# Optimization experiments

Measured on AMD Instinct MI355X. Metric: run time of the kernel, lower is better.

## Reference

```python
import jax, jax.numpy as jnp
import numpy as np

B, C, H, W = 8, 256, 64, 64
N = 3  # num_param
EPS = 1e-5


def conv2d(x, w, b=None, stride=(1, 1), padding=((0, 0), (0, 0)), dilation=(1, 1), groups=1):
    out = jax.lax.conv_general_dilated(
        x, w, window_strides=stride, padding=padding, rhs_dilation=dilation,
        dimension_numbers=('NCHW', 'OIHW', 'NCHW'), feature_group_count=groups)
    if b is not None:
        out = out + b[None, :, None, None]
    return out


def akconv(x, p_w, p_b, ak_w, ak_gamma, ak_beta):
    b, c, h, w = x.shape
    offset = conv2d(x, p_w, p_b, padding=((1, 1), (1, 1)))  # (b, 2N, h, w)
    # initial kernel offsets p_n for num_param=3: rows [0,0,1], cols [0,1,0]
    p_n = jnp.concatenate([jnp.array([0., 0., 1.]), jnp.array([0., 1., 0.])]).reshape(1, 2 * N, 1, 1)
    gx = jnp.broadcast_to(jnp.arange(h, dtype=x.dtype)[:, None], (h, w))
    gy = jnp.broadcast_to(jnp.arange(w, dtype=x.dtype)[None, :], (h, w))
    p_0 = jnp.concatenate([jnp.tile(gx[None, None], (1, N, 1, 1)),
                           jnp.tile(gy[None, None], (1, N, 1, 1))], axis=1)  # (1, 2N, h, w)
    p = p_0 + p_n + offset                      # (b, 2N, h, w)
    p = jnp.transpose(p, (0, 2, 3, 1))          # (b, h, w, 2N)
    q = jnp.floor(jax.lax.stop_gradient(p))
    q_lt_x = jnp.clip(q[..., :N], 0, h - 1)
    q_lt_y = jnp.clip(q[..., N:], 0, w - 1)
    q_rb_x = jnp.clip(q[..., :N] + 1, 0, h - 1)
    q_rb_y = jnp.clip(q[..., N:] + 1, 0, w - 1)
    px = jnp.clip(p[..., :N], 0, h - 1)
    py = jnp.clip(p[..., N:], 0, w - 1)
    # bilinear weights (b, h, w, N)
    g_lt = (1 + (q_lt_x - px)) * (1 + (q_lt_y - py))
    g_rb = (1 - (q_rb_x - px)) * (1 - (q_rb_y - py))
    g_lb = (1 + (q_lt_x - px)) * (1 - (q_rb_y - py))
    g_rt = (1 - (q_rb_x - px)) * (1 + (q_lt_y - py))

    x_flat = x.reshape(b, c, h * w)

    def gather(qx, qy):
        idx = (qx * w + qy).astype(jnp.int32).reshape(b, -1)  # (b, h*w*N)
        out = jnp.take_along_axis(x_flat, idx[:, None, :], axis=2)
        return out.reshape(b, c, h, w, N)

    x_off = (g_lt[:, None] * gather(q_lt_x, q_lt_y)
             + g_rb[:, None] * gather(q_rb_x, q_rb_y)
             + g_lb[:, None] * gather(q_lt_x, q_rb_y)
             + g_rt[:, None] * gather(q_rb_x, q_lt_y))   # (b, c, h, w, N)
    # rearrange 'b c h w n -> b c (h n) w'
    x_off = jnp.transpose(x_off, (0, 1, 2, 4, 3)).reshape(b, c, h * N, w)
    out = conv2d(x_off, ak_w, None, stride=(N, 1))        # (b, c, h, w)
    # BatchNorm2d in training mode (batch statistics) + SiLU
    mean = out.mean(axis=(0, 2, 3), keepdims=True)
    var = ((out - mean) ** 2).mean(axis=(0, 2, 3), keepdims=True)
    out = (out - mean) / jnp.sqrt(var + EPS) * ak_gamma[None, :, None, None] + ak_beta[None, :, None, None]
    return jax.nn.silu(out)


def lka(x, w0, b0, ws, bs, w1, b1):
    u = x
    attn = conv2d(x, w0, b0, padding=((2, 2), (2, 2)), groups=C)                       # 5x5 depthwise
    attn = conv2d(attn, ws, bs, padding=((9, 9), (9, 9)), dilation=(3, 3), groups=C)   # 7x7 dw, dil 3
    attn = conv2d(attn, w1, b1)                                                        # 1x1
    return u * attn


def setup_inputs() -> dict:
    key = jax.random.key(0)
    ks = jax.random.split(key, 8)
    return {
        'x': jax.random.normal(ks[0], (B, C, H, W), jnp.float32),
        'p_w': jax.random.normal(ks[1], (2 * N, C, 3, 3), jnp.float32) * 0.01,
        'p_b': jnp.zeros((2 * N,), jnp.float32),
        'ak_w': jax.random.normal(ks[2], (C, C, 3, 1), jnp.float32) * 0.05,
        'ak_gamma': jnp.ones((C,), jnp.float32),
        'ak_beta': jnp.zeros((C,), jnp.float32),
        'lka0_w': jax.random.normal(ks[3], (C, 1, 5, 5), jnp.float32) * 0.05,
        'lka0_b': jnp.zeros((C,), jnp.float32),
        'lkas_w': jax.random.normal(ks[4], (C, 1, 7, 7), jnp.float32) * 0.05,
        'lkas_b': jnp.zeros((C,), jnp.float32),
        'lka1_w': jax.random.normal(ks[5], (C, C, 1, 1), jnp.float32) * 0.05,
        'lka1_b': jnp.zeros((C,), jnp.float32),
        'conv_w': jax.random.normal(ks[6], (C, C, 1, 1), jnp.float32) * 0.05,
        'conv_b': jnp.zeros((C,), jnp.float32),
    }


def reference(x, p_w, p_b, ak_w, ak_gamma, ak_beta, lka0_w, lka0_b, lkas_w, lkas_b, lka1_w, lka1_b, conv_w, conv_b):
    res = x
    y = akconv(x, p_w, p_b, ak_w, ak_gamma, ak_beta)
    y = lka(y, lka0_w, lka0_b, lkas_w, lkas_b, lka1_w, lka1_b)
    y = conv2d(y, conv_w, conv_b)
    return y + res
```

## Files before the change

kernel.cpp:

```cpp
#include <hip/hip_runtime.h>
#include <math.h>
#include <stdint.h>

#define B_ 8
#define C_ 256
#define HW_ 4096
#define NPIX 32768
#define NELEM (B_*C_*HW_)

typedef __attribute__((ext_vector_type(8))) short short8;
typedef __attribute__((ext_vector_type(4))) float f32x4;

__device__ __forceinline__ unsigned short f2bf(float f) {
    union { float f; uint32_t u; } v; v.f = f;
    uint32_t r = v.u + 0x7FFFu + ((v.u >> 16) & 1u);
    return (unsigned short)(r >> 16);
}
__device__ __forceinline__ float b2f(unsigned short h) {
    union { uint32_t u; float f; } v; v.u = ((uint32_t)h) << 16; return v.f;
}
__device__ __forceinline__ float silu_f(float v) { return v / (1.f + __expf(-v)); }

__global__ __launch_bounds__(256) void prep_kernel(
    const float* __restrict__ akw, const float* __restrict__ l1w,
    const float* __restrict__ cvw, const float* __restrict__ pw,
    unsigned short* __restrict__ wak, unsigned short* __restrict__ wl1,
    unsigned short* __restrict__ wcv, float* __restrict__ pwt)
{
    int gid = blockIdx.x * 256 + threadIdx.x;
    if (gid < 196608) {
        unsigned co = (unsigned)gid / 768u;
        unsigned kp = (unsigned)gid - co * 768u;
        unsigned n = kp >> 8, ci = kp & 255;
        wak[gid] = f2bf(akw[co * 768 + ci * 3 + n]);
    }
    else if (gid < 262144) { int g = gid - 196608; wl1[g] = f2bf(l1w[g]); }
    else if (gid < 327680) { int g = gid - 262144; wcv[g] = f2bf(cvw[g]); }
    else if (gid < 346112) {
        int idx = gid - 327680;
        int ci = idx / 72, r = idx - ci * 72;
        int tt = r / 12, t9 = r - tt * 12;
        pwt[idx] = (t9 < 9) ? pw[tt * 2304 + ci * 9 + t9] : 0.f;
    }
}

__global__ __launch_bounds__(256) void transpose_kernel(
    const float* __restrict__ x, float* __restrict__ xt)
{
    int blk = blockIdx.x;
    int b = blk & 7;
    int rest = blk >> 3;
    int half = rest & 1, i = rest >> 1;
    int bi = b * 64 + i;
    int tid = threadIdx.x;
    __shared__ float tile[64 * 132];

    {
        int ci_l = tid >> 6, jj = tid & 63;
        const float* ip = x + ((size_t)b * C_ + half * 128 + ci_l) * HW_ + i * 64 + jj;
        #pragma unroll 4
        for (int it = 0; it < 32; ++it)
            tile[jj * 132 + ci_l + it * 4] = ip[(size_t)it * 4 * HW_];
    }
    __syncthreads();
    {
        int j = tid >> 2, q = tid & 3;
        float* op = xt + ((size_t)(bi * 64 + j)) * 256 + half * 128 + q * 32;
        #pragma unroll
        for (int f = 0; f < 8; ++f)
            *(float4*)(op + f * 4) = *(const float4*)&tile[j * 132 + q * 32 + f * 4];
    }
}

__global__ __launch_bounds__(256) void offset_s1_kernel(
    const float* __restrict__ x, const float* __restrict__ pwt,
    float* __restrict__ part)
{
    int blk = blockIdx.x;
    int b = blk & 7;
    int rest = blk >> 3;
    int g = rest & 7, i = rest >> 3;
    int bi = b * 64 + i;
    int tid = threadIdx.x;

    __shared__ float tile[6600];

    {
        int cs = tid >> 3, r8 = tid & 7;
        const float* xp = x + ((size_t)b * C_ + g * 32 + cs) * HW_;
        #pragma unroll
        for (int t = 0; t < 6; ++t) {
            int idx = r8 * 6 + t;
            int r = idx >> 4, v4 = idx & 15;
            int ii = i + r - 1;
            float4 val = make_float4(0.f, 0.f, 0.f, 0.f);
            if (ii >= 0 && ii < 64)
                val = *(const float4*)(xp + ii * 64 + v4 * 4);
            int base = (r * 66 + 1 + v4 * 4) * 33 + cs;
            tile[base]      = val.x;  tile[base + 33]  = val.y;
            tile[base + 66] = val.z;  tile[base + 99]  = val.w;
        }
        if (tid < 192) {
            int ci = tid / 6, rem = tid - ci * 6;
            int ki = rem >> 1, side = rem & 1;
            tile[(ki * 66 + side * 65) * 33 + ci] = 0.f;
        }
    }
    __syncthreads();

    int sub = tid >> 4;
    int jq  = tid & 15;

    float acc[6][4];
    #pragma unroll
    for (int tt = 0; tt < 6; ++tt)
        #pragma unroll
        for (int p = 0; p < 4; ++p) acc[tt][p] = 0.f;

    #pragma unroll
    for (int t = 0; t < 2; ++t) {
        int ci = sub + 16 * t;
        float xv[3][6];
        #pragma unroll
        for (int ki = 0; ki < 3; ++ki)
            #pragma unroll
            for (int cc = 0; cc < 6; ++cc)
                xv[ki][cc] = tile[(ki * 66 + jq * 4 + cc) * 33 + ci];
        const float* wp = pwt + (g * 32 + ci) * 72;
        #pragma unroll
        for (int tt = 0; tt < 6; ++tt) {
            float w[9];
            *(float4*)&w[0] = *(const float4*)(wp + tt * 12);
            *(float4*)&w[4] = *(const float4*)(wp + tt * 12 + 4);
            w[8] = wp[tt * 12 + 8];
            #pragma unroll
            for (int ki = 0; ki < 3; ++ki)
                #pragma unroll
                for (int kj = 0; kj < 3; ++kj) {
                    float wgt = w[ki * 3 + kj];
                    #pragma unroll
                    for (int p = 0; p < 4; ++p)
                        acc[tt][p] += wgt * xv[ki][kj + p];
                }
        }
    }

    __syncthreads();
    {
        float* s2 = tile + sub * 387;
        #pragma unroll
        for (int tt = 0; tt < 6; ++tt)
            #pragma unroll
            for (int p = 0; p < 4; ++p)
                s2[tt * 64 + jq * 4 + p] = acc[tt][p];
    }
    __syncthreads();
    size_t pslot = (size_t)bi * 8 + g;
    for (int idx = tid; idx < 384; idx += 256) {
        float s = 0.f;
        #pragma unroll
        for (int sb = 0; sb < 16; ++sb)
            s += tile[sb * 387 + idx];
        part[pslot * 384 + idx] = s;
    }
}

__global__ __launch_bounds__(256) void offset_s2_kernel(
    const float* __restrict__ part, const float* __restrict__ pb,
    int2* __restrict__ tbl_off, float4* __restrict__ tbl_w)
{
    int pix = blockIdx.x * 256 + threadIdx.x;
    int b = pix >> 12, rem = pix & 4095, i = rem >> 6, j = rem & 63;
    int bi = b * 64 + i;
    float v[6];
    #pragma unroll
    for (int tt = 0; tt < 6; ++tt) v[tt] = pb[tt];
    for (int g = 0; g < 8; ++g) {
        const float* pp = part + ((size_t)bi * 8 + g) * 384;
        #pragma unroll
        for (int tt = 0; tt < 6; ++tt) v[tt] += pp[tt * 64 + j];
    }
    const float pnx[3] = {0.f, 0.f, 1.f};
    const float pny[3] = {0.f, 1.f, 0.f};
    #pragma unroll
    for (int n = 0; n < 3; ++n) {
        float px_ = (float)i + pnx[n] + v[n];
        float py_ = (float)j + pny[n] + v[n + 3];
        float qx = floorf(px_), qy = floorf(py_);
        float qlx = fminf(fmaxf(qx,       0.f), 63.f);
        float qly = fminf(fmaxf(qy,       0.f), 63.f);
        float qrx = fminf(fmaxf(qx + 1.f, 0.f), 63.f);
        float qry = fminf(fmaxf(qy + 1.f, 0.f), 63.f);
        float pxc = fminf(fmaxf(px_,      0.f), 63.f);
        float pyc = fminf(fmaxf(py_,      0.f), 63.f);
        float glt = (1.f + (qlx - pxc)) * (1.f + (qly - pyc));
        float grb = (1.f - (qrx - pxc)) * (1.f - (qry - pyc));
        float glb = (1.f + (qlx - pxc)) * (1.f - (qry - pyc));
        float grt = (1.f - (qrx - pxc)) * (1.f + (qly - pyc));
        int ilx = (int)qlx, irx = (int)qrx;
        int ily = (int)qly, iry = (int)qry;
        int c0; float a0, a1, b0, b1;
        if (ily == iry) {
            if (ily == 0) { c0 = 0;  a0 = glt + glb; a1 = 0.f; b0 = grt + grb; b1 = 0.f; }
            else          { c0 = 62; a0 = 0.f; a1 = glt + glb; b0 = 0.f; b1 = grt + grb; }
        } else { c0 = ily; a0 = glt; a1 = glb; b0 = grt; b1 = grb; }
        int oi = (b * 3 + n) * HW_ + i * 64 + j;
        tbl_off[oi] = make_int2(ilx * 64 + c0, irx * 64 + c0);
        tbl_w[oi]   = make_float4(a0, a1, b0, b1);
    }
}

__global__ __launch_bounds__(256) void gather_kernel(
    const float* __restrict__ xt, const int2* __restrict__ tbl_off,
    const float4* __restrict__ tbl_w, unsigned short* __restrict__ v)
{
    int blk = blockIdx.x;
    int b = blk & 7;
    int rest = blk >> 3;
    int n = rest >> 6, i = rest & 63;
    int bi = b * 64 + i;
    int tid = threadIdx.x;
    int lane = tid & 63, wv = tid >> 6;
    int ci4 = lane * 4;
    const float* xb = xt + (size_t)b * 1048576;

    for (int it0 = 0; it0 < 16; it0 += 4) {
        float4 A[4], Bv[4], Cv[4], Dv[4], w4[4];
        #pragma unroll
        for (int u = 0; u < 4; ++u) {
            int j = wv * 16 + it0 + u;
            int oi = (b * 3 + n) * HW_ + i * 64 + j;
            int2 off = tbl_off[oi];
            w4[u] = tbl_w[oi];
            const float* p0 = xb + (size_t)off.x * 256 + ci4;
            const float* p1 = xb + (size_t)off.y * 256 + ci4;
            A[u]  = *(const float4*)p0;
            Bv[u] = *(const float4*)(p0 + 256);
            Cv[u] = *(const float4*)p1;
            Dv[u] = *(const float4*)(p1 + 256);
        }
        #pragma unroll
        for (int u = 0; u < 4; ++u) {
            int j = wv * 16 + it0 + u;
            int pix = bi * 64 + j;
            union { unsigned short h[4]; uint2 q; } pk;
            pk.h[0] = f2bf(w4[u].x*A[u].x + w4[u].y*Bv[u].x + w4[u].z*Cv[u].x + w4[u].w*Dv[u].x);
            pk.h[1] = f2bf(w4[u].x*A[u].y + w4[u].y*Bv[u].y + w4[u].z*Cv[u].y + w4[u].w*Dv[u].y);
            pk.h[2] = f2bf(w4[u].x*A[u].z + w4[u].y*Bv[u].z + w4[u].z*Cv[u].z + w4[u].w*Dv[u].z);
            pk.h[3] = f2bf(w4[u].x*A[u].w + w4[u].y*Bv[u].w + w4[u].z*Cv[u].w + w4[u].w*Dv[u].w);
            *(uint2*)&v[(size_t)pix * 768 + n * 256 + ci4] = pk.q;
        }
    }
}

__global__ __launch_bounds__(256) void ak_mfma_kernel(
    const unsigned short* __restrict__ v, const unsigned short* __restrict__ W,
    unsigned short* __restrict__ yh, float* __restrict__ p1, float* __restrict__ p2)
{
    int blk = blockIdx.x;
    int b = blk & 7, i = blk >> 3;
    int tid = threadIdx.x;
    int wv = tid >> 6, lane = tid & 63;
    int quad = lane >> 4, l15 = lane & 15;
    __shared__ __align__(16) unsigned short sA[8192];
    __shared__ __align__(16) unsigned short sB[2048];
    int pixS = tid & 63, kqS = tid >> 6;
    int pix0 = (b * 64 + i) * 64;

    f32x4 acc[4][4];
    #pragma unroll
    for (int mt = 0; mt < 4; ++mt)
        #pragma unroll
        for (int nt = 0; nt < 4; ++nt) acc[mt][nt] = (f32x4){0.f, 0.f, 0.f, 0.f};

    for (int k0 = 0; k0 < 768; k0 += 32) {
        #pragma unroll
        for (int s = 0; s < 4; ++s) {
            int co = tid;
            *(uint4*)&sA[(s * 256 + co) * 8] =
                *(const uint4*)&W[co * 768 + k0 + s * 8];
        }
        *(uint4*)&sB[(kqS * 64 + pixS) * 8] =
            *(const uint4*)&v[(size_t)(pix0 + pixS) * 768 + k0 + kqS * 8];
        __syncthreads();
        short8 af[4], bf[4];
        #pragma unroll
        for (int mt = 0; mt < 4; ++mt)
            af[mt] = *(const short8*)&sA[(quad * 256 + wv * 64 + mt * 16 + l15) * 8];
        #pragma unroll
        for (int nt = 0; nt < 4; ++nt)
            bf[nt] = *(const short8*)&sB[(quad * 64 + nt * 16 + l15) * 8];
        #pragma unroll
        for (int mt = 0; mt < 4; ++mt)
            #pragma unroll
            for (int nt = 0; nt < 4; ++nt)
                acc[mt][nt] = __builtin_amdgcn_mfma_f32_16x16x32_bf16(
                    af[mt], bf[nt], acc[mt][nt], 0, 0, 0);
        __syncthreads();
    }
    #pragma unroll
    for (int mt = 0; mt < 4; ++mt) {
        #pragma unroll
        for (int r = 0; r < 4; ++r) {
            int co = wv * 64 + mt * 16 + quad * 4 + r;
            size_t base = ((size_t)b * C_ + co) * HW_ + i * 64;
            float s1 = 0.f, s2 = 0.f;
            #pragma unroll
            for (int nt = 0; nt < 4; ++nt) {
                float val = acc[mt][nt][r];
                s1 += val; s2 += val * val;
                yh[base + nt * 16 + l15] = f2bf(val);
            }
            #pragma unroll
            for (int m = 1; m < 16; m <<= 1) {
                s1 += __shfl_xor(s1, m); s2 += __shfl_xor(s2, m);
            }
            if (l15 == 0) { p1[co * 512 + blk] = s1; p2[co * 512 + blk] = s2; }
        }
    }
}

__global__ __launch_bounds__(256) void bn_stats_kernel(
    const float* __restrict__ p1, const float* __restrict__ p2,
    const float* __restrict__ gamma, const float* __restrict__ beta,
    float* __restrict__ ss)
{
    int co = blockIdx.x, tid = threadIdx.x;
    float a = p1[co * 512 + tid] + p1[co * 512 + 256 + tid];
    float q = p2[co * 512 + tid] + p2[co * 512 + 256 + tid];
    __shared__ float r1[256], r2[256];
    r1[tid] = a; r2[tid] = q; __syncthreads();
    for (int st = 128; st > 0; st >>= 1) {
        if (tid < st) { r1[tid] += r1[tid + st]; r2[tid] += r2[tid + st]; }
        __syncthreads();
    }
    if (tid == 0) {
        const float inv_n = 1.f / (float)NPIX;
        float m = r1[0] * inv_n;
        float var = r2[0] * inv_n - m * m;
        float sc = gamma[co] * rsqrtf(var + 1e-5f);
        ss[co] = sc; ss[256 + co] = beta[co] - m * sc;
    }
}

__global__ __launch_bounds__(256) void dw5_fused_kernel(
    const unsigned short* __restrict__ in, const float* __restrict__ ss,
    const float* __restrict__ w, const float* __restrict__ bias,
    unsigned short* __restrict__ out)
{
    int blkI = blockIdx.x;
    int b = blkI & 7, c = blkI >> 3;
    int bc = b * 256 + c;
    int tid = threadIdx.x;
    __shared__ float tile[68 * 68];
    float sc = ss[c], sh = ss[256 + c];
    const unsigned short* ip = in + (size_t)bc * HW_;
    for (int s = tid; s < 68 * 68; s += 256) {
        int r = s / 68, cc = s - r * 68;
        int ii = r - 2, jj = cc - 2;
        float vv = 0.f;
        if (ii >= 0 && ii < 64 && jj >= 0 && jj < 64) {
            float t = b2f(ip[ii * 64 + jj]) * sc + sh;
            vv = silu_f(t);
        }
        tile[s] = vv;
    }
    float wr[25];
    #pragma unroll
    for (int t = 0; t < 25; ++t) wr[t] = w[c * 25 + t];
    float bv = bias[c];
    __syncthreads();
    int j0 = (tid & 15) * 4, ig = tid >> 4;
    unsigned short* op = out + (size_t)bc * HW_;
    for (int r = 0; r < 4; ++r) {
        int i = r * 16 + ig;
        float o0 = bv, o1 = bv, o2 = bv, o3 = bv;
        #pragma unroll
        for (int di = 0; di < 5; ++di) {
            const float* tp = &tile[(i + di) * 68 + j0];
            float4 a = *(const float4*)tp;
            float4 bq = *(const float4*)(tp + 4);
            float vv[8] = {a.x, a.y, a.z, a.w, bq.x, bq.y, bq.z, bq.w};
            #pragma unroll
            for (int dj = 0; dj < 5; ++dj) {
                float wv = wr[di * 5 + dj];
                o0 += wv * vv[dj];     o1 += wv * vv[dj + 1];
                o2 += wv * vv[dj + 2]; o3 += wv * vv[dj + 3];
            }
        }
        union { unsigned short h[4]; uint2 u; } pk;
        pk.h[0] = f2bf(o0); pk.h[1] = f2bf(o1);
        pk.h[2] = f2bf(o2); pk.h[3] = f2bf(o3);
        *(uint2*)&op[i * 64 + j0] = pk.u;
    }
}

__global__ __launch_bounds__(256) void dw7d3_kernel(
    const unsigned short* __restrict__ in, const float* __restrict__ w,
    const float* __restrict__ bias, unsigned short* __restrict__ out)
{
    int blkI = blockIdx.x;
    int b = blkI & 7, c = blkI >> 3;
    int bc = b * 256 + c;
    int tid = threadIdx.x;
    __shared__ float tile[82 * 84];
    const unsigned short* ip = in + (size_t)bc * HW_;
    for (int s = tid; s < 82 * 84; s += 256) {
        int r = s / 84, cc = s - r * 84;
        int ii = r - 9, jj = cc - 9;
        float vv = 0.f;
        if (ii >= 0 && ii < 64 && jj >= 0 && jj < 64) vv = b2f(ip[ii * 64 + jj]);
        tile[s] = vv;
    }
    float wr[49];
    #pragma unroll
    for (int t = 0; t < 49; ++t) wr[t] = w[c * 49 + t];
    float bv = bias[c];
    __syncthreads();
    int j0 = (tid & 15) * 4, ig = tid >> 4;
    unsigned short* op = out + (size_t)bc * HW_;
    for (int r = 0; r < 4; ++r) {
        int i = r * 16 + ig;
        float o0 = bv, o1 = bv, o2 = bv, o3 = bv;
        #pragma unroll
        for (int di = 0; di < 7; ++di) {
            const float* tp = &tile[(i + 3 * di) * 84 + j0];
            float vv[24];
            #pragma unroll
            for (int q = 0; q < 6; ++q)
                *(float4*)&vv[q * 4] = *(const float4*)(tp + q * 4);
            #pragma unroll
            for (int dj = 0; dj < 7; ++dj) {
                float wv = wr[di * 7 + dj];
                o0 += wv * vv[3 * dj];     o1 += wv * vv[3 * dj + 1];
                o2 += wv * vv[3 * dj + 2]; o3 += wv * vv[3 * dj + 3];
            }
        }
        union { unsigned short h[4]; uint2 u; } pk;
        pk.h[0] = f2bf(o0); pk.h[1] = f2bf(o1);
        pk.h[2] = f2bf(o2); pk.h[3] = f2bf(o3);
        *(uint2*)&op[i * 64 + j0] = pk.u;
    }
}

template<int MODE>
__global__ __launch_bounds__(256) void gemm1x1_mfma(
    const unsigned short* __restrict__ in, const unsigned short* __restrict__ W,
    const float* __restrict__ bias,
    const unsigned short* __restrict__ auxh, const float* __restrict__ auxf,
    const float* __restrict__ ss,
    unsigned short* __restrict__ out_bf, float* __restrict__ out_f)
{
    int blk = blockIdx.x;
    int b = blk & 7, i = blk >> 3;
    int tid = threadIdx.x;
    int wv = tid >> 6, lane = tid & 63;
    int quad = lane >> 4, l15 = lane & 15;
    __shared__ __align__(16) unsigned short sA[8192];
    __shared__ __align__(16) unsigned short sB[2048];
    int pixS = tid & 63, kqS = tid >> 6;

    f32x4 acc[4][4];
    #pragma unroll
    for (int mt = 0; mt < 4; ++mt)
        #pragma unroll
        for (int nt = 0; nt < 4; ++nt) acc[mt][nt] = (f32x4){0.f, 0.f, 0.f, 0.f};

    for (int k0 = 0; k0 < 256; k0 += 32) {
        #pragma unroll
        for (int s = 0; s < 4; ++s) {
            int co = tid;
            *(uint4*)&sA[(s * 256 + co) * 8] =
                *(const uint4*)&W[co * 256 + k0 + s * 8];
        }
        {
            const unsigned short* vp =
                in + ((size_t)b * C_ + k0 + kqS * 8) * HW_ + i * 64 + pixS;
            union { unsigned short h[8]; uint4 u; } hb;
            #pragma unroll
            for (int jj = 0; jj < 8; ++jj) hb.h[jj] = vp[(size_t)jj * HW_];
            *(uint4*)&sB[(kqS * 64 + pixS) * 8] = hb.u;
        }
        __syncthreads();
        short8 af[4], bf[4];
        #pragma unroll
        for (int mt = 0; mt < 4; ++mt)
            af[mt] = *(const short8*)&sA[(quad * 256 + wv * 64 + mt * 16 + l15) * 8];
        #pragma unroll
        for (int nt = 0; nt < 4; ++nt)
            bf[nt] = *(const short8*)&sB[(quad * 64 + nt * 16 + l15) * 8];
        #pragma unroll
        for (int mt = 0; mt < 4; ++mt)
            #pragma unroll
            for (int nt = 0; nt < 4; ++nt)
                acc[mt][nt] = __builtin_amdgcn_mfma_f32_16x16x32_bf16(
                    af[mt], bf[nt], acc[mt][nt], 0, 0, 0);
        __syncthreads();
    }
    #pragma unroll
    for (int mt = 0; mt < 4; ++mt) {
        #pragma unroll
        for (int r = 0; r < 4; ++r) {
            int co = wv * 64 + mt * 16 + quad * 4 + r;
            float bco = bias[co];
            size_t base = ((size_t)b * C_ + co) * HW_ + i * 64;
            if (MODE == 0) {
                float sc = ss[co], sh = ss[256 + co];
                #pragma unroll
                for (int nt = 0; nt < 4; ++nt) {
                    int col = nt * 16 + l15;
                    float o = acc[mt][nt][r] + bco;
                    float u = silu_f(b2f(auxh[base + col]) * sc + sh);
                    out_bf[base + col] = f2bf(o * u);
                }
            } else {
                #pragma unroll
                for (int nt = 0; nt < 4; ++nt) {
                    int col = nt * 16 + l15;
                    out_f[base + col] = acc[mt][nt][r] + bco + auxf[base + col];
                }
            }
        }
    }
}

extern "C" void kernel_launch(void* const* d_in, const int* in_sizes, int n_in,
                              void* d_out, int out_size, void* d_ws, size_t ws_size,
                              hipStream_t stream) {
    const float* x     = (const float*)d_in[0];
    const float* p_w   = (const float*)d_in[1];
    const float* p_b   = (const float*)d_in[2];
    const float* ak_w  = (const float*)d_in[3];
    const float* ak_g  = (const float*)d_in[4];
    const float* ak_b  = (const float*)d_in[5];
    const float* l0_w  = (const float*)d_in[6];
    const float* l0_b  = (const float*)d_in[7];
    const float* ls_w  = (const float*)d_in[8];
    const float* ls_b  = (const float*)d_in[9];
    const float* l1_w  = (const float*)d_in[10];
    const float* l1_b  = (const float*)d_in[11];
    const float* cv_w  = (const float*)d_in[12];
    const float* cv_b  = (const float*)d_in[13];
    float* out = (float*)d_out;

    char* w = (char*)d_ws;
    int2*   tbl_off = (int2*)w;
    float4* tbl_w   = (float4*)(w + 786432);
    unsigned short* wak = (unsigned short*)(w + 2359296);
    unsigned short* wl1 = (unsigned short*)(w + 2752512);
    unsigned short* wcv = (unsigned short*)(w + 2883584);
    float* p1 = (float*)(w + 3014656);
    float* p2 = (float*)(w + 3538944);
    float* ss = (float*)(w + 4063232);
    float* pwt = (float*)(w + 4065280);
    float* xt   = (float*)(w + 4194304);
    unsigned short* ybh    = (unsigned short*)(w + 4194304);
    unsigned short* dw5out = (unsigned short*)(w + 20971520);
    float* part = (float*)(w + 37748736);
    unsigned short* attn   = (unsigned short*)(w + 37748736);
    unsigned short* v      = (unsigned short*)(w + 44040192);
    unsigned short* g0out  = (unsigned short*)(w + 54525952);

    prep_kernel<<<1352, 256, 0, stream>>>(ak_w, l1_w, cv_w, p_w, wak, wl1, wcv, pwt);
    offset_s1_kernel<<<4096, 256, 0, stream>>>(x, pwt, part);
    offset_s2_kernel<<<128, 256, 0, stream>>>(part, p_b, tbl_off, tbl_w);
    transpose_kernel<<<1024, 256, 0, stream>>>(x, xt);
    gather_kernel<<<1536, 256, 0, stream>>>(xt, tbl_off, tbl_w, v);
    ak_mfma_kernel<<<512, 256, 0, stream>>>(v, wak, ybh, p1, p2);
    bn_stats_kernel<<<256, 256, 0, stream>>>(p1, p2, ak_g, ak_b, ss);
    dw5_fused_kernel<<<2048, 256, 0, stream>>>(ybh, ss, l0_w, l0_b, dw5out);
    dw7d3_kernel<<<2048, 256, 0, stream>>>(dw5out, ls_w, ls_b, attn);
    gemm1x1_mfma<0><<<512, 256, 0, stream>>>(attn, wl1, l1_b, ybh, nullptr, ss, g0out, nullptr);
    gemm1x1_mfma<1><<<512, 256, 0, stream>>>(g0out, wcv, cv_b, nullptr, x, nullptr, nullptr, out);
}
```

Before: 316.8 us.

## Double-buffer GEMM tiles with direct global-to-LDS loads in AK and 1x1 kernels

Converts the AK-conv GEMM and the 1x1 GEMM kernels to a double-buffered LDS pipeline. Each loop iteration now issues the next K-slice while MFMAs run on the current one, using global_load_lds to copy weights (and AK activations) straight into shared memory without going through registers. The 1x1 kernel keeps a register-staged strided B load that is written to LDS after the compute. This doubles LDS use per block, which may lower occupancy, and depends on the LDS layout produced by the per-wave global_load_lds matching the old indexing.

Result: slower. 342.1 us (+8.0%).

```diff
diff --git a/kernel.cpp b/kernel.cpp
--- a/kernel.cpp
+++ b/kernel.cpp
@@ -20,6 +20,18 @@
     union { uint32_t u; float f; } v; v.u = ((uint32_t)h) << 16; return v.f;
 }
 __device__ __forceinline__ float silu_f(float v) { return v / (1.f + __expf(-v)); }
+
+__device__ __forceinline__ void gl2lds16(const void* g, void* l) {
+    __builtin_amdgcn_global_load_lds(
+        (const __attribute__((address_space(1))) void*)g,
+        (__attribute__((address_space(3))) void*)l,
+        16, 0, 0);
+}
+__device__ __forceinline__ void pipeline_barrier() {
+    asm volatile("s_waitcnt vmcnt(0) lgkmcnt(0)" ::: "memory");
+    __builtin_amdgcn_s_barrier();
+    asm volatile("" ::: "memory");
+}
 
 __global__ __launch_bounds__(256) void prep_kernel(
     const float* __restrict__ akw, const float* __restrict__ l1w,
@@ -262,41 +274,47 @@
     int tid = threadIdx.x;
     int wv = tid >> 6, lane = tid & 63;
     int quad = lane >> 4, l15 = lane & 15;
-    __shared__ __align__(16) unsigned short sA[8192];
-    __shared__ __align__(16) unsigned short sB[2048];
-    int pixS = tid & 63, kqS = tid >> 6;
+    __shared__ __align__(16) unsigned short sA[2][8192];
+    __shared__ __align__(16) unsigned short sB[2][2048];
     int pix0 = (b * 64 + i) * 64;
 
+    const unsigned short* wp = W + (size_t)(wv * 64 + lane) * 768;
+    const unsigned short* vp = v + (size_t)(pix0 + lane) * 768;
+
     f32x4 acc[4][4];
     #pragma unroll
     for (int mt = 0; mt < 4; ++mt)
         #pragma unroll
         for (int nt = 0; nt < 4; ++nt) acc[mt][nt] = (f32x4){0.f, 0.f, 0.f, 0.f};
 
-    for (int k0 = 0; k0 < 768; k0 += 32) {
-        #pragma unroll
-        for (int s = 0; s < 4; ++s) {
-            int co = tid;
-            *(uint4*)&sA[(s * 256 + co) * 8] =
-                *(const uint4*)&W[co * 768 + k0 + s * 8];
-        }
-        *(uint4*)&sB[(kqS * 64 + pixS) * 8] =
-            *(const uint4*)&v[(size_t)(pix0 + pixS) * 768 + k0 + kqS * 8];
-        __syncthreads();
+    auto stage = [&](int bb, int k0) {
+        #pragma unroll
+        for (int s = 0; s < 4; ++s)
+            gl2lds16(wp + k0 + s * 8, &sA[bb][(s * 256 + wv * 64) * 8]);
+        gl2lds16(vp + k0 + wv * 8, &sB[bb][(wv * 64) * 8]);
+    };
+
+    stage(0, 0);
+    pipeline_barrier();
+    int cur = 0;
+    #pragma unroll 2
+    for (int t = 0; t < 24; ++t) {
+        if (t < 23) stage(cur ^ 1, (t + 1) * 32);
         short8 af[4], bf[4];
         #pragma unroll
         for (int mt = 0; mt < 4; ++mt)
-            af[mt] = *(const short8*)&sA[(quad * 256 + wv * 64 + mt * 16 + l15) * 8];
+            af[mt] = *(const short8*)&sA[cur][(quad * 256 + wv * 64 + mt * 16 + l15) * 8];
         #pragma unroll
         for (int nt = 0; nt < 4; ++nt)
-            bf[nt] = *(const short8*)&sB[(quad * 64 + nt * 16 + l15) * 8];
+            bf[nt] = *(const short8*)&sB[cur][(quad * 64 + nt * 16 + l15) * 8];
         #pragma unroll
         for (int mt = 0; mt < 4; ++mt)
             #pragma unroll
             for (int nt = 0; nt < 4; ++nt)
                 acc[mt][nt] = __builtin_amdgcn_mfma_f32_16x16x32_bf16(
                     af[mt], bf[nt], acc[mt][nt], 0, 0, 0);
-        __syncthreads();
+        pipeline_barrier();
+        cur ^= 1;
     }
     #pragma unroll
     for (int mt = 0; mt < 4; ++mt) {
@@ -456,46 +474,61 @@
     int tid = threadIdx.x;
     int wv = tid >> 6, lane = tid & 63;
     int quad = lane >> 4, l15 = lane & 15;
-    __shared__ __align__(16) unsigned short sA[8192];
-    __shared__ __align__(16) unsigned short sB[2048];
+    __shared__ __align__(16) unsigned short sA[2][8192];
+    __shared__ __align__(16) unsigned short sB[2][2048];
     int pixS = tid & 63, kqS = tid >> 6;
 
+    const unsigned short* wp = W + (size_t)(wv * 64 + lane) * 256;
+    const unsigned short* bp = in + ((size_t)b * C_) * HW_ + i * 64 + pixS;
+
     f32x4 acc[4][4];
     #pragma unroll
     for (int mt = 0; mt < 4; ++mt)
         #pragma unroll
         for (int nt = 0; nt < 4; ++nt) acc[mt][nt] = (f32x4){0.f, 0.f, 0.f, 0.f};
 
-    for (int k0 = 0; k0 < 256; k0 += 32) {
-        #pragma unroll
-        for (int s = 0; s < 4; ++s) {
-            int co = tid;
-            *(uint4*)&sA[(s * 256 + co) * 8] =
-                *(const uint4*)&W[co * 256 + k0 + s * 8];
-        }
-        {
-            const unsigned short* vp =
-                in + ((size_t)b * C_ + k0 + kqS * 8) * HW_ + i * 64 + pixS;
-            union { unsigned short h[8]; uint4 u; } hb;
-            #pragma unroll
-            for (int jj = 0; jj < 8; ++jj) hb.h[jj] = vp[(size_t)jj * HW_];
-            *(uint4*)&sB[(kqS * 64 + pixS) * 8] = hb.u;
-        }
-        __syncthreads();
+    auto stageA = [&](int bb, int k0) {
+        #pragma unroll
+        for (int s = 0; s < 4; ++s)
+            gl2lds16(wp + k0 + s * 8, &sA[bb][(s * 256 + wv * 64) * 8]);
+    };
+    union U8 { unsigned short h[8]; uint4 u; };
+    auto loadB = [&](U8& hb, int k0) {
+        const unsigned short* p = bp + (size_t)(k0 + kqS * 8) * HW_;
+        #pragma unroll
+        for (int jj = 0; jj < 8; ++jj) hb.h[jj] = p[(size_t)jj * HW_];
+    };
+
+    U8 hb;
+    stageA(0, 0);
+    loadB(hb, 0);
+    asm volatile("s_waitcnt vmcnt(0)" ::: "memory");
+    *(uint4*)&sB[0][(kqS * 64 + pixS) * 8] = hb.u;
+    pipeline_barrier();
+
+    int cur = 0;
+    #pragma unroll 2
+    for (int t = 0; t < 8; ++t) {
+        if (t < 7) { stageA(cur ^ 1, (t + 1) * 32); loadB(hb, (t + 1) * 32); }
         short8 af[4], bf[4];
         #pragma unroll
         for (int mt = 0; mt < 4; ++mt)
-            af[mt] = *(const short8*)&sA[(quad * 256 + wv * 64 + mt * 16 + l15) * 8];
+            af[mt] = *(const short8*)&sA[cur][(quad * 256 + wv * 64 + mt * 16 + l15) * 8];
         #pragma unroll
         for (int nt = 0; nt < 4; ++nt)
-            bf[nt] = *(const short8*)&sB[(quad * 64 + nt * 16 + l15) * 8];
+            bf[nt] = *(const short8*)&sB[cur][(quad * 64 + nt * 16 + l15) * 8];
         #pragma unroll
         for (int mt = 0; mt < 4; ++mt)
             #pragma unroll
             for (int nt = 0; nt < 4; ++nt)
                 acc[mt][nt] = __builtin_amdgcn_mfma_f32_16x16x32_bf16(
                     af[mt], bf[nt], acc[mt][nt], 0, 0, 0);
-        __syncthreads();
+        if (t < 7) {
+            asm volatile("s_waitcnt vmcnt(0)" ::: "memory");
+            *(uint4*)&sB[cur ^ 1][(kqS * 64 + pixS) * 8] = hb.u;
+        }
+        pipeline_barrier();
+        cur ^= 1;
     }
     #pragma unroll
     for (int mt = 0; mt < 4; ++mt) {
```

## Split GEMM output channels across two blocks and load tiles via global_load_lds

Applied to the files above, without the earlier changes.

Each MFMA GEMM kernel (the AKConv 768-K GEMM and both 1x1 GEMMs) now covers half the output channels per block, which doubles the grid from 512 to 1024 blocks and halves accumulator registers and weight LDS. The weight and activation tile loads switch to direct global-to-LDS transfers, which skip the VGPR round-trip. The aim is better occupancy and latency hiding on a 256-CU part. In exchange, the B tile (pixels) is now loaded twice across the two blocks, and per-block MFMA work per sync is halved.

After: 326.1 us. 2.9% more time.

```diff
diff --git a/kernel.cpp b/kernel.cpp
--- a/kernel.cpp
+++ b/kernel.cpp
@@ -20,6 +20,13 @@
     union { uint32_t u; float f; } v; v.u = ((uint32_t)h) << 16; return v.f;
 }
 __device__ __forceinline__ float silu_f(float v) { return v / (1.f + __expf(-v)); }
+
+__device__ __forceinline__ void gl2lds16(const void* g, void* l) {
+    __builtin_amdgcn_global_load_lds(
+        (const __attribute__((address_space(1))) void*)g,
+        (__attribute__((address_space(3))) void*)l,
+        16, 0, 0);
+}
 
 __global__ __launch_bounds__(256) void prep_kernel(
     const float* __restrict__ akw, const float* __restrict__ l1w,
@@ -258,40 +265,45 @@
     unsigned short* __restrict__ yh, float* __restrict__ p1, float* __restrict__ p2)
 {
     int blk = blockIdx.x;
-    int b = blk & 7, i = blk >> 3;
+    int mt2 = blk & 1;
+    int rest = blk >> 1;
+    int b = rest & 7, i = rest >> 3;
     int tid = threadIdx.x;
     int wv = tid >> 6, lane = tid & 63;
     int quad = lane >> 4, l15 = lane & 15;
-    __shared__ __align__(16) unsigned short sA[8192];
+    __shared__ __align__(16) unsigned short sA[4096];
     __shared__ __align__(16) unsigned short sB[2048];
+    int pix0 = (b * 64 + i) * 64;
+    int co0 = mt2 * 128;
+
+    int coS = tid & 127, shS = tid >> 7;
     int pixS = tid & 63, kqS = tid >> 6;
-    int pix0 = (b * 64 + i) * 64;
-
-    f32x4 acc[4][4];
-    #pragma unroll
-    for (int mt = 0; mt < 4; ++mt)
+    const unsigned short* wpA = W + (size_t)(co0 + coS) * 768;
+    const unsigned short* vpB = v + (size_t)(pix0 + pixS) * 768;
+
+    f32x4 acc[2][4];
+    #pragma unroll
+    for (int mt = 0; mt < 2; ++mt)
         #pragma unroll
         for (int nt = 0; nt < 4; ++nt) acc[mt][nt] = (f32x4){0.f, 0.f, 0.f, 0.f};
 
     for (int k0 = 0; k0 < 768; k0 += 32) {
         #pragma unroll
-        for (int s = 0; s < 4; ++s) {
-            int co = tid;
-            *(uint4*)&sA[(s * 256 + co) * 8] =
-                *(const uint4*)&W[co * 768 + k0 + s * 8];
-        }
-        *(uint4*)&sB[(kqS * 64 + pixS) * 8] =
-            *(const uint4*)&v[(size_t)(pix0 + pixS) * 768 + k0 + kqS * 8];
+        for (int q = 0; q < 2; ++q) {
+            int s = shS * 2 + q;
+            gl2lds16(wpA + k0 + s * 8, &sA[(s * 128 + coS) * 8]);
+        }
+        gl2lds16(vpB + k0 + kqS * 8, &sB[(kqS * 64 + pixS) * 8]);
         __syncthreads();
-        short8 af[4], bf[4];
-        #pragma unroll
-        for (int mt = 0; mt < 4; ++mt)
-            af[mt] = *(const short8*)&sA[(quad * 256 + wv * 64 + mt * 16 + l15) * 8];
+        short8 af[2], bf[4];
+        #pragma unroll
+        for (int mt = 0; mt < 2; ++mt)
+            af[mt] = *(const short8*)&sA[(quad * 128 + wv * 32 + mt * 16 + l15) * 8];
         #pragma unroll
         for (int nt = 0; nt < 4; ++nt)
             bf[nt] = *(const short8*)&sB[(quad * 64 + nt * 16 + l15) * 8];
         #pragma unroll
-        for (int mt = 0; mt < 4; ++mt)
+        for (int mt = 0; mt < 2; ++mt)
             #pragma unroll
             for (int nt = 0; nt < 4; ++nt)
                 acc[mt][nt] = __builtin_amdgcn_mfma_f32_16x16x32_bf16(
@@ -299,10 +311,10 @@
         __syncthreads();
     }
     #pragma unroll
-    for (int mt = 0; mt < 4; ++mt) {
+    for (int mt = 0; mt < 2; ++mt) {
         #pragma unroll
         for (int r = 0; r < 4; ++r) {
-            int co = wv * 64 + mt * 16 + quad * 4 + r;
+            int co = co0 + wv * 32 + mt * 16 + quad * 4 + r;
             size_t base = ((size_t)b * C_ + co) * HW_ + i * 64;
             float s1 = 0.f, s2 = 0.f;
             #pragma unroll
@@ -315,7 +327,7 @@
             for (int m = 1; m < 16; m <<= 1) {
                 s1 += __shfl_xor(s1, m); s2 += __shfl_xor(s2, m);
             }
-            if (l15 == 0) { p1[co * 512 + blk] = s1; p2[co * 512 + blk] = s2; }
+            if (l15 == 0) { p1[co * 512 + rest] = s1; p2[co * 512 + rest] = s2; }
         }
     }
 }
@@ -452,45 +464,50 @@
     unsigned short* __restrict__ out_bf, float* __restrict__ out_f)
 {
     int blk = blockIdx.x;
-    int b = blk & 7, i = blk >> 3;
+    int mt2 = blk & 1;
+    int rest = blk >> 1;
+    int b = rest & 7, i = rest >> 3;
     int tid = threadIdx.x;
     int wv = tid >> 6, lane = tid & 63;
     int quad = lane >> 4, l15 = lane & 15;
-    __shared__ __align__(16) unsigned short sA[8192];
+    __shared__ __align__(16) unsigned short sA[4096];
     __shared__ __align__(16) unsigned short sB[2048];
+    int co0 = mt2 * 128;
+
+    int coS = tid & 127, shS = tid >> 7;
     int pixS = tid & 63, kqS = tid >> 6;
-
-    f32x4 acc[4][4];
-    #pragma unroll
-    for (int mt = 0; mt < 4; ++mt)
+    const unsigned short* wpA = W + (size_t)(co0 + coS) * 256;
+    const unsigned short* bp = in + ((size_t)b * C_) * HW_ + i * 64 + pixS;
+
+    f32x4 acc[2][4];
+    #pragma unroll
+    for (int mt = 0; mt < 2; ++mt)
         #pragma unroll
         for (int nt = 0; nt < 4; ++nt) acc[mt][nt] = (f32x4){0.f, 0.f, 0.f, 0.f};
 
     for (int k0 = 0; k0 < 256; k0 += 32) {
         #pragma unroll
-        for (int s = 0; s < 4; ++s) {
-            int co = tid;
-            *(uint4*)&sA[(s * 256 + co) * 8] =
-                *(const uint4*)&W[co * 256 + k0 + s * 8];
+        for (int q = 0; q < 2; ++q) {
+            int s = shS * 2 + q;
+            gl2lds16(wpA + k0 + s * 8, &sA[(s * 128 + coS) * 8]);
         }
         {
-            const unsigned short* vp =
-                in + ((size_t)b * C_ + k0 + kqS * 8) * HW_ + i * 64 + pixS;
+            const unsigned short* p = bp + (size_t)(k0 + kqS * 8) * HW_;
             union { unsigned short h[8]; uint4 u; } hb;
             #pragma unroll
-            for (int jj = 0; jj < 8; ++jj) hb.h[jj] = vp[(size_t)jj * HW_];
+            for (int jj = 0; jj < 8; ++jj) hb.h[jj] = p[(size_t)jj * HW_];
             *(uint4*)&sB[(kqS * 64 + pixS) * 8] = hb.u;
         }
         __syncthreads();
-        short8 af[4], bf[4];
-        #pragma unroll
-        for (int mt = 0; mt < 4; ++mt)
-            af[mt] = *(const short8*)&sA[(quad * 256 + wv * 64 + mt * 16 + l15) * 8];
+        short8 af[2], bf[4];
+        #pragma unroll
+        for (int mt = 0; mt < 2; ++mt)
+            af[mt] = *(const short8*)&sA[(quad * 128 + wv * 32 + mt * 16 + l15) * 8];
         #pragma unroll
         for (int nt = 0; nt < 4; ++nt)
             bf[nt] = *(const short8*)&sB[(quad * 64 + nt * 16 + l15) * 8];
         #pragma unroll
-        for (int mt = 0; mt < 4; ++mt)
+        for (int mt = 0; mt < 2; ++mt)
             #pragma unroll
             for (int nt = 0; nt < 4; ++nt)
                 acc[mt][nt] = __builtin_amdgcn_mfma_f32_16x16x32_bf16(
@@ -498,10 +515,10 @@
         __syncthreads();
     }
     #pragma unroll
-    for (int mt = 0; mt < 4; ++mt) {
+    for (int mt = 0; mt < 2; ++mt) {
         #pragma unroll
         for (int r = 0; r < 4; ++r) {
-            int co = wv * 64 + mt * 16 + quad * 4 + r;
+            int co = co0 + wv * 32 + mt * 16 + quad * 4 + r;
             float bco = bias[co];
             size_t base = ((size_t)b * C_ + co) * HW_ + i * 64;
             if (MODE == 0) {
@@ -566,10 +583,10 @@
     offset_s2_kernel<<<128, 256, 0, stream>>>(part, p_b, tbl_off, tbl_w);
     transpose_kernel<<<1024, 256, 0, stream>>>(x, xt);
     gather_kernel<<<1536, 256, 0, stream>>>(xt, tbl_off, tbl_w, v);
-    ak_mfma_kernel<<<512, 256, 0, stream>>>(v, wak, ybh, p1, p2);
+    ak_mfma_kernel<<<1024, 256, 0, stream>>>(v, wak, ybh, p1, p2);
     bn_stats_kernel<<<256, 256, 0, stream>>>(p1, p2, ak_g, ak_b, ss);
     dw5_fused_kernel<<<2048, 256, 0, stream>>>(ybh, ss, l0_w, l0_b, dw5out);
     dw7d3_kernel<<<2048, 256, 0, stream>>>(dw5out, ls_w, ls_b, attn);
-    gemm1x1_mfma<0><<<512, 256, 0, stream>>>(attn, wl1, l1_b, ybh, nullptr, ss, g0out, nullptr);
-    gemm1x1_mfma<1><<<512, 256, 0, stream>>>(g0out, wcv, cv_b, nullptr, x, nullptr, nullptr, out);
-}
+    gemm1x1_mfma<0><<<1024, 256, 0, stream>>>(attn, wl1, l1_b, ybh, nullptr, ss, g0out, nullptr);
+    gemm1x1_mfma<1><<<1024, 256, 0, stream>>>(g0out, wcv, cv_b, nullptr, x, nullptr, nullptr, out);
+}
```

## Pre-tile weights and gather output for direct global-to-LDS loads in GEMMs

Applied to the files above, without the earlier changes.

Weights are now stored in a k-chunk-major tiled layout, and the gather kernel writes its bf16 output already tiled per row-block in the GEMM's shared-memory order. The AK and 1x1 GEMM kernels then fill LDS with global_load_lds 16-byte direct loads instead of staging through registers. This aims to cut VGPR traffic and instruction count in the load phase and to make the loads contiguous. It relies on global_load_lds with 16-byte width being supported on this target, and makes the intermediate layout specific to these kernels.

New measurement: 305.1 us. 3.7% less time.

```diff
diff --git a/kernel.cpp b/kernel.cpp
--- a/kernel.cpp
+++ b/kernel.cpp
@@ -21,6 +21,13 @@
 }
 __device__ __forceinline__ float silu_f(float v) { return v / (1.f + __expf(-v)); }
 
+__device__ __forceinline__ void gl2lds16(const void* g, void* l) {
+    __builtin_amdgcn_global_load_lds(
+        (const __attribute__((address_space(1))) void*)g,
+        (__attribute__((address_space(3))) void*)l,
+        16, 0, 0);
+}
+
 __global__ __launch_bounds__(256) void prep_kernel(
     const float* __restrict__ akw, const float* __restrict__ l1w,
     const float* __restrict__ cvw, const float* __restrict__ pw,
@@ -29,13 +36,23 @@
 {
     int gid = blockIdx.x * 256 + threadIdx.x;
     if (gid < 196608) {
-        unsigned co = (unsigned)gid / 768u;
-        unsigned kp = (unsigned)gid - co * 768u;
-        unsigned n = kp >> 8, ci = kp & 255;
+        int e = gid & 7;
+        int co = (gid >> 3) & 255;
+        int q = gid >> 11;
+        int kpp = q * 8 + e;
+        int n = kpp >> 8, ci = kpp & 255;
         wak[gid] = f2bf(akw[co * 768 + ci * 3 + n]);
     }
-    else if (gid < 262144) { int g = gid - 196608; wl1[g] = f2bf(l1w[g]); }
-    else if (gid < 327680) { int g = gid - 262144; wcv[g] = f2bf(cvw[g]); }
+    else if (gid < 262144) {
+        int g = gid - 196608;
+        int e = g & 7, co = (g >> 3) & 255, q = g >> 11;
+        wl1[g] = f2bf(l1w[co * 256 + q * 8 + e]);
+    }
+    else if (gid < 327680) {
+        int g = gid - 262144;
+        int e = g & 7, co = (g >> 3) & 255, q = g >> 11;
+        wcv[g] = f2bf(cvw[co * 256 + q * 8 + e]);
+    }
     else if (gid < 346112) {
         int idx = gid - 327680;
         int ci = idx / 72, r = idx - ci * 72;
@@ -224,6 +241,11 @@
     int ci4 = lane * 4;
     const float* xb = xt + (size_t)b * 1048576;
 
+    int tC = (n << 3) + (ci4 >> 5);
+    int kq = (ci4 >> 3) & 3;
+    int e  = ci4 & 7;
+    unsigned short* vb = v + ((size_t)bi * 24 + tC) * 2048 + kq * 512 + e;
+
     for (int it0 = 0; it0 < 16; it0 += 4) {
         float4 A[4], Bv[4], Cv[4], Dv[4], w4[4];
         #pragma unroll
@@ -242,13 +264,12 @@
         #pragma unroll
         for (int u = 0; u < 4; ++u) {
             int j = wv * 16 + it0 + u;
-            int pix = bi * 64 + j;
             union { unsigned short h[4]; uint2 q; } pk;
             pk.h[0] = f2bf(w4[u].x*A[u].x + w4[u].y*Bv[u].x + w4[u].z*Cv[u].x + w4[u].w*Dv[u].x);
             pk.h[1] = f2bf(w4[u].x*A[u].y + w4[u].y*Bv[u].y + w4[u].z*Cv[u].y + w4[u].w*Dv[u].y);
             pk.h[2] = f2bf(w4[u].x*A[u].z + w4[u].y*Bv[u].z + w4[u].z*Cv[u].z + w4[u].w*Dv[u].z);
             pk.h[3] = f2bf(w4[u].x*A[u].w + w4[u].y*Bv[u].w + w4[u].z*Cv[u].w + w4[u].w*Dv[u].w);
-            *(uint2*)&v[(size_t)pix * 768 + n * 256 + ci4] = pk.q;
+            *(uint2*)&vb[j * 8] = pk.q;
         }
     }
 }
@@ -259,13 +280,14 @@
 {
     int blk = blockIdx.x;
     int b = blk & 7, i = blk >> 3;
+    int P = b * 64 + i;
     int tid = threadIdx.x;
     int wv = tid >> 6, lane = tid & 63;
     int quad = lane >> 4, l15 = lane & 15;
     __shared__ __align__(16) unsigned short sA[8192];
     __shared__ __align__(16) unsigned short sB[2048];
-    int pixS = tid & 63, kqS = tid >> 6;
-    int pix0 = (b * 64 + i) * 64;
+
+    const unsigned short* vP = v + (size_t)P * 24 * 2048;
 
     f32x4 acc[4][4];
     #pragma unroll
@@ -273,15 +295,11 @@
         #pragma unroll
         for (int nt = 0; nt < 4; ++nt) acc[mt][nt] = (f32x4){0.f, 0.f, 0.f, 0.f};
 
-    for (int k0 = 0; k0 < 768; k0 += 32) {
-        #pragma unroll
-        for (int s = 0; s < 4; ++s) {
-            int co = tid;
-            *(uint4*)&sA[(s * 256 + co) * 8] =
-                *(const uint4*)&W[co * 768 + k0 + s * 8];
-        }
-        *(uint4*)&sB[(kqS * 64 + pixS) * 8] =
-            *(const uint4*)&v[(size_t)(pix0 + pixS) * 768 + k0 + kqS * 8];
+    for (int t = 0; t < 24; ++t) {
+        #pragma unroll
+        for (int s = 0; s < 4; ++s)
+            gl2lds16(W + ((size_t)(t * 4 + s) * 256 + tid) * 8, &sA[(s * 256 + tid) * 8]);
+        gl2lds16(vP + (size_t)t * 2048 + tid * 8, &sB[tid * 8]);
         __syncthreads();
         short8 af[4], bf[4];
         #pragma unroll
@@ -460,25 +478,23 @@
     __shared__ __align__(16) unsigned short sB[2048];
     int pixS = tid & 63, kqS = tid >> 6;
 
+    const unsigned short* bp = in + ((size_t)b * C_) * HW_ + i * 64 + pixS;
+
     f32x4 acc[4][4];
     #pragma unroll
     for (int mt = 0; mt < 4; ++mt)
         #pragma unroll
         for (int nt = 0; nt < 4; ++nt) acc[mt][nt] = (f32x4){0.f, 0.f, 0.f, 0.f};
 
-    for (int k0 = 0; k0 < 256; k0 += 32) {
-        #pragma unroll
-        for (int s = 0; s < 4; ++s) {
-            int co = tid;
-            *(uint4*)&sA[(s * 256 + co) * 8] =
-                *(const uint4*)&W[co * 256 + k0 + s * 8];
-        }
+    for (int t = 0; t < 8; ++t) {
+        #pragma unroll
+        for (int s = 0; s < 4; ++s)
+            gl2lds16(W + ((size_t)(t * 4 + s) * 256 + tid) * 8, &sA[(s * 256 + tid) * 8]);
         {
-            const unsigned short* vp =
-                in + ((size_t)b * C_ + k0 + kqS * 8) * HW_ + i * 64 + pixS;
+            const unsigned short* p = bp + (size_t)(t * 32 + kqS * 8) * HW_;
             union { unsigned short h[8]; uint4 u; } hb;
             #pragma unroll
-            for (int jj = 0; jj < 8; ++jj) hb.h[jj] = vp[(size_t)jj * HW_];
+            for (int jj = 0; jj < 8; ++jj) hb.h[jj] = p[(size_t)jj * HW_];
             *(uint4*)&sB[(kqS * 64 + pixS) * 8] = hb.u;
         }
         __syncthreads();
```
